# Kernel optimization log

Measured on AMD Instinct MI355X. Metric: run time of the kernel, lower is better.

Reference implementation:

```python
import jax, jax.numpy as jnp
import numpy as np

B, TX, D = 32, 4096, 512  # D = 2*units


def setup_inputs() -> dict:
    key = jax.random.key(0)
    ks = jax.random.split(key, 8)
    return {
        "a": jax.random.normal(ks[0], (B, TX, D), dtype=jnp.float32),
        "h": jax.random.normal(ks[1], (B, D), dtype=jnp.float32),
        "coverage": jax.random.uniform(ks[2], (B, TX, 1), dtype=jnp.float32),
        "X_mask": jax.random.randint(ks[3], (B, TX, 1), 0, 2).astype(bool),
        "Wa": jax.random.normal(ks[4], (D, D), dtype=jnp.float32) * 0.02,
        "Wh": jax.random.normal(ks[5], (D, D), dtype=jnp.float32) * 0.02,
        "Wc": jax.random.normal(ks[6], (1, D), dtype=jnp.float32) * 0.02,
        "V": jax.random.normal(ks[7], (D, 1), dtype=jnp.float32) * 0.02,
        "use_coverage": 1,
        "use_masking": 1,
    }


def reference(a, h, coverage, X_mask, Wa, Wh, Wc, V, use_coverage, use_masking):
    # h repeated over Tx (RepeatVector): [B, Tx, D]
    enc = jnp.einsum('btd,de->bte', a, Wa)
    dec = jnp.einsum('bd,de->be', h, Wh)[:, None, :]  # broadcast over Tx
    features = enc + dec
    if use_coverage:
        features = features + jnp.einsum('btc,ce->bte', coverage, Wc)
    e = jnp.einsum('bte,eo->bto', jnp.tanh(features), V)  # [B, Tx, 1]
    # NB: softmax over last axis of size 1 -> all ones (faithful to source)
    alpha = jax.nn.softmax(e, axis=-1)
    if use_masking:
        alpha = jnp.where(X_mask, alpha, jnp.zeros_like(alpha))
        alpha_sum = jnp.sum(alpha, axis=1)            # [B, 1]
        alpha = jnp.squeeze(alpha, axis=-1) / alpha_sum  # [B, Tx]
        alpha = alpha[..., None]                      # [B, Tx, 1]
    context = jnp.sum(alpha * a, axis=1, keepdims=True)  # [B, 1, D]
    return context, jnp.squeeze(alpha, axis=-1)
```

## Files before the change

### kernel.cpp

```cpp
#include <hip/hip_runtime.h>

#define BB 32
#define TXX 4096
#define DD 512

__global__ __launch_bounds__(256) void k_alpha(const void* __restrict__ mask_raw,
                                               const int* __restrict__ use_masking_p,
                                               float* __restrict__ alpha_out)
{
    __shared__ int s_has_f, s_has_odd;
    __shared__ float s_red[256];
    const int b = blockIdx.x;
    const int tid = threadIdx.x;

    if (tid == 0) { s_has_f = 0; s_has_odd = 0; }
    __syncthreads();
    {
        unsigned int w = ((const unsigned int*)mask_raw)[tid];
        if (w == 0x3F800000u) atomicOr(&s_has_f, 1);
        else if (w > 1u)      atomicOr(&s_has_odd, 1);
    }
    __syncthreads();
    const int fmt = s_has_f ? 2 : (s_has_odd ? 1 : 0);
    const int use_masking = (use_masking_p[0] != 0);

    const unsigned char* mb = (const unsigned char*)mask_raw;
    const int*           mi = (const int*)mask_raw;
    const float*         mf = (const float*)mask_raw;

    bool m[16];
    float cnt = 0.f;
    #pragma unroll
    for (int k = 0; k < 16; ++k) {
        const int t = b * TXX + tid + k * 256;
        bool mm;
        if (fmt == 1)      mm = (mb[t] != 0);
        else if (fmt == 0) mm = (mi[t] != 0);
        else               mm = (mf[t] != 0.f);
        m[k] = mm;
        cnt += mm ? 1.f : 0.f;
    }
    s_red[tid] = cnt;
    __syncthreads();
    for (int s = 128; s > 0; s >>= 1) {
        if (tid < s) s_red[tid] += s_red[tid + s];
        __syncthreads();
    }
    const float inv = use_masking ? (1.f / s_red[0]) : 1.f;

    #pragma unroll
    for (int k = 0; k < 16; ++k) {
        const int t = tid + k * 256;
        float w = use_masking ? (m[k] ? inv : 0.f) : 1.f;
        alpha_out[b * TXX + t] = w;
    }
}

__global__ __launch_bounds__(256) void k_partial(const float* __restrict__ a,
                                                 const float* __restrict__ alpha,
                                                 float4* __restrict__ part,
                                                 int tc_count)
{
    const int b    = blockIdx.y;
    const int tc   = blockIdx.x;
    const int tid  = threadIdx.x;
    const int d4   = tid & 127;
    const int tsub = tid >> 7;
    const int tchunk = TXX / tc_count;
    const int t0 = tc * tchunk;

    __shared__ float          s_w[256];
    __shared__ unsigned short s_idx[256];
    __shared__ int            s_wtot[4];
    __shared__ float4         s_acc[128];

    const float* al = alpha + (size_t)b * TXX;

    {
        const int lane = tid & 63;
        const int wave = tid >> 6;
        float w = 0.f;
        bool p = false;
        if (tid < tchunk) { w = al[t0 + tid]; p = (w != 0.f); }
        unsigned long long bal = __ballot(p);
        int lpfx = __popcll(bal & ((lane == 0) ? 0ull : (~0ull >> (64 - lane))));
        if (lane == 0) s_wtot[wave] = __popcll(bal);
        __syncthreads();
        int woff = 0;
        for (int i = 0; i < wave; ++i) woff += s_wtot[i];
        if (p) {
            int pos = woff + lpfx;
            s_idx[pos] = (unsigned short)tid;
            s_w[pos]   = w;
        }
        __syncthreads();
    }
    const int n = s_wtot[0] + s_wtot[1] + s_wtot[2] + s_wtot[3];

    const float4* a4 = (const float4*)(a + (size_t)b * TXX * DD);
    float4 acc = {0.f, 0.f, 0.f, 0.f};
    #pragma unroll 4
    for (int j = tsub; j < n; j += 2) {
        const int t = t0 + s_idx[j];
        const float w = s_w[j];
        float4 v = a4[(size_t)t * (DD / 4) + d4];
        acc.x += w * v.x; acc.y += w * v.y;
        acc.z += w * v.z; acc.w += w * v.w;
    }

    if (tsub == 1) s_acc[d4] = acc;
    __syncthreads();
    if (tsub == 0) {
        float4 o = s_acc[d4];
        acc.x += o.x; acc.y += o.y; acc.z += o.z; acc.w += o.w;
        part[((size_t)b * tc_count + tc) * 128 + d4] = acc;
    }
}

__global__ __launch_bounds__(256) void k_reduce(const float4* __restrict__ part,
                                                float4* __restrict__ ctx,
                                                int tc_count)
{
    const int gid = blockIdx.x * 256 + threadIdx.x;
    const int b   = gid >> 7;
    const int d4  = gid & 127;
    float4 acc = {0.f, 0.f, 0.f, 0.f};
    for (int tc = 0; tc < tc_count; ++tc) {
        float4 v = part[((size_t)b * tc_count + tc) * 128 + d4];
        acc.x += v.x; acc.y += v.y; acc.z += v.z; acc.w += v.w;
    }
    ctx[gid] = acc;
}

extern "C" void kernel_launch(void* const* d_in, const int* in_sizes, int n_in,
                              void* d_out, int out_size, void* d_ws, size_t ws_size,
                              hipStream_t stream) {
    const float* a          = (const float*)d_in[0];
    const void*  mask       = d_in[3];
    const int*   use_mask_p = (const int*)d_in[9];

    float* out   = (float*)d_out;
    float* alpha = out + BB * DD;

    int tc_count = 32;
    while (tc_count > 16 && (size_t)BB * tc_count * 128 * 16 > ws_size) tc_count >>= 1;

    k_alpha  <<<BB, 256, 0, stream>>>(mask, use_mask_p, alpha);
    k_partial<<<dim3(tc_count, BB), 256, 0, stream>>>(a, alpha, (float4*)d_ws, tc_count);
    k_reduce <<<(BB * 128) / 256, 256, 0, stream>>>((const float4*)d_ws, (float4*)out, tc_count);
}
```

Before: 360.6 us.

## Fuse alpha computation into partial-sum kernel, redundantly counting mask per block

Merges the alpha kernel into the partial reduction kernel. Each block now recomputes the per-batch mask count on its own, writes its chunk of alpha, and compacts the indices from the mask directly instead of reading alpha back. The normalization factor is applied once after accumulation rather than per element. This removes one kernel launch and the alpha round trip, at the cost of every one of the 32 blocks per batch re-reading the whole 4096-element mask row. The workspace-size fallback for the chunk count is also dropped, so TC is fixed at 32.

```diff
diff --git a/kernel.cpp b/kernel.cpp
--- a/kernel.cpp
+++ b/kernel.cpp
@@ -3,15 +3,26 @@
 #define BB 32
 #define TXX 4096
 #define DD 512
+#define TC 32
+#define TCHUNK (TXX / TC)
 
-__global__ __launch_bounds__(256) void k_alpha(const void* __restrict__ mask_raw,
-                                               const int* __restrict__ use_masking_p,
-                                               float* __restrict__ alpha_out)
+__global__ __launch_bounds__(256) void k_main(const float* __restrict__ a,
+                                              const void* __restrict__ mask_raw,
+                                              const int* __restrict__ use_masking_p,
+                                              float* __restrict__ alpha_out,
+                                              float4* __restrict__ part)
 {
-    __shared__ int s_has_f, s_has_odd;
-    __shared__ float s_red[256];
-    const int b = blockIdx.x;
-    const int tid = threadIdx.x;
+    const int b    = blockIdx.y;
+    const int tc   = blockIdx.x;
+    const int tid  = threadIdx.x;
+    const int lane = tid & 63;
+    const int wave = tid >> 6;
+
+    __shared__ int            s_has_f, s_has_odd;
+    __shared__ float          s_red[256];
+    __shared__ unsigned short s_idx[TCHUNK];
+    __shared__ int            s_wcnt[2];
+    __shared__ float4         s_acc[128];
 
     if (tid == 0) { s_has_f = 0; s_has_odd = 0; }
     __syncthreads();
@@ -28,7 +39,6 @@
     const int*           mi = (const int*)mask_raw;
     const float*         mf = (const float*)mask_raw;
 
-    bool m[16];
     float cnt = 0.f;
     #pragma unroll
     for (int k = 0; k < 16; ++k) {
@@ -37,7 +47,6 @@
         if (fmt == 1)      mm = (mb[t] != 0);
         else if (fmt == 0) mm = (mi[t] != 0);
         else               mm = (mf[t] != 0.f);
-        m[k] = mm;
         cnt += mm ? 1.f : 0.f;
     }
     s_red[tid] = cnt;
@@ -48,85 +57,60 @@
     }
     const float inv = use_masking ? (1.f / s_red[0]) : 1.f;
 
-    #pragma unroll
-    for (int k = 0; k < 16; ++k) {
-        const int t = tid + k * 256;
-        float w = use_masking ? (m[k] ? inv : 0.f) : 1.f;
-        alpha_out[b * TXX + t] = w;
+    const int t0 = tc * TCHUNK;
+    bool p = false;
+    if (tid < TCHUNK) {
+        const int t = b * TXX + t0 + tid;
+        bool mm;
+        if (fmt == 1)      mm = (mb[t] != 0);
+        else if (fmt == 0) mm = (mi[t] != 0);
+        else               mm = (mf[t] != 0.f);
+        p = use_masking ? mm : true;
+        alpha_out[(size_t)b * TXX + t0 + tid] =
+            use_masking ? (mm ? inv : 0.f) : 1.f;
     }
-}
+    unsigned long long bal = __ballot(p);
+    int lpfx = __popcll(bal & ((lane == 0) ? 0ull : (~0ull >> (64 - lane))));
+    if (lane == 0 && wave < 2) s_wcnt[wave] = __popcll(bal);
+    __syncthreads();
+    if (p) {
+        int pos = (wave == 1 ? s_wcnt[0] : 0) + lpfx;
+        s_idx[pos] = (unsigned short)tid;
+    }
+    __syncthreads();
+    const int n = s_wcnt[0] + s_wcnt[1];
 
-__global__ __launch_bounds__(256) void k_partial(const float* __restrict__ a,
-                                                 const float* __restrict__ alpha,
-                                                 float4* __restrict__ part,
-                                                 int tc_count)
-{
-    const int b    = blockIdx.y;
-    const int tc   = blockIdx.x;
-    const int tid  = threadIdx.x;
     const int d4   = tid & 127;
     const int tsub = tid >> 7;
-    const int tchunk = TXX / tc_count;
-    const int t0 = tc * tchunk;
-
-    __shared__ float          s_w[256];
-    __shared__ unsigned short s_idx[256];
-    __shared__ int            s_wtot[4];
-    __shared__ float4         s_acc[128];
-
-    const float* al = alpha + (size_t)b * TXX;
-
-    {
-        const int lane = tid & 63;
-        const int wave = tid >> 6;
-        float w = 0.f;
-        bool p = false;
-        if (tid < tchunk) { w = al[t0 + tid]; p = (w != 0.f); }
-        unsigned long long bal = __ballot(p);
-        int lpfx = __popcll(bal & ((lane == 0) ? 0ull : (~0ull >> (64 - lane))));
-        if (lane == 0) s_wtot[wave] = __popcll(bal);
-        __syncthreads();
-        int woff = 0;
-        for (int i = 0; i < wave; ++i) woff += s_wtot[i];
-        if (p) {
-            int pos = woff + lpfx;
-            s_idx[pos] = (unsigned short)tid;
-            s_w[pos]   = w;
-        }
-        __syncthreads();
-    }
-    const int n = s_wtot[0] + s_wtot[1] + s_wtot[2] + s_wtot[3];
-
-    const float4* a4 = (const float4*)(a + (size_t)b * TXX * DD);
+    const float4* a4 = (const float4*)(a + (size_t)b * TXX * DD)
+                     + (size_t)t0 * (DD / 4);
     float4 acc = {0.f, 0.f, 0.f, 0.f};
     #pragma unroll 4
     for (int j = tsub; j < n; j += 2) {
-        const int t = t0 + s_idx[j];
-        const float w = s_w[j];
-        float4 v = a4[(size_t)t * (DD / 4) + d4];
-        acc.x += w * v.x; acc.y += w * v.y;
-        acc.z += w * v.z; acc.w += w * v.w;
+        float4 v = a4[(size_t)s_idx[j] * (DD / 4) + d4];
+        acc.x += v.x; acc.y += v.y; acc.z += v.z; acc.w += v.w;
     }
 
     if (tsub == 1) s_acc[d4] = acc;
     __syncthreads();
     if (tsub == 0) {
         float4 o = s_acc[d4];
-        acc.x += o.x; acc.y += o.y; acc.z += o.z; acc.w += o.w;
-        part[((size_t)b * tc_count + tc) * 128 + d4] = acc;
+        acc.x = (acc.x + o.x) * inv; acc.y = (acc.y + o.y) * inv;
+        acc.z = (acc.z + o.z) * inv; acc.w = (acc.w + o.w) * inv;
+        part[((size_t)b * TC + tc) * 128 + d4] = acc;
     }
 }
 
 __global__ __launch_bounds__(256) void k_reduce(const float4* __restrict__ part,
-                                                float4* __restrict__ ctx,
-                                                int tc_count)
+                                                float4* __restrict__ ctx)
 {
     const int gid = blockIdx.x * 256 + threadIdx.x;
     const int b   = gid >> 7;
     const int d4  = gid & 127;
     float4 acc = {0.f, 0.f, 0.f, 0.f};
-    for (int tc = 0; tc < tc_count; ++tc) {
-        float4 v = part[((size_t)b * tc_count + tc) * 128 + d4];
+    #pragma unroll
+    for (int tc = 0; tc < TC; ++tc) {
+        float4 v = part[((size_t)b * TC + tc) * 128 + d4];
         acc.x += v.x; acc.y += v.y; acc.z += v.z; acc.w += v.w;
     }
     ctx[gid] = acc;
@@ -142,10 +126,8 @@
     float* out   = (float*)d_out;
     float* alpha = out + BB * DD;
 
-    int tc_count = 32;
-    while (tc_count > 16 && (size_t)BB * tc_count * 128 * 16 > ws_size) tc_count >>= 1;
-
-    k_alpha  <<<BB, 256, 0, stream>>>(mask, use_mask_p, alpha);
-    k_partial<<<dim3(tc_count, BB), 256, 0, stream>>>(a, alpha, (float4*)d_ws, tc_count);
-    k_reduce <<<(BB * 128) / 256, 256, 0, stream>>>((const float4*)d_ws, (float4*)out, tc_count);
+    k_main  <<<dim3(TC, BB), 256, 0, stream>>>(a, mask, use_mask_p, alpha,
+                                               (float4*)d_ws);
+    k_reduce<<<(BB * 128) / 256, 256, 0, stream>>>((const float4*)d_ws,
+                                                   (float4*)out);
 }
```

Measured after the change: 352.1 us. 1.02x faster.
